# Kernel optimization log

Measured on AMD Instinct MI355X. Metric: run time of the kernel, lower is better.

Reference implementation:

```python
import jax, jax.numpy as jnp
import numpy as np

D_MODEL = 1024; N_HEAD = 16; HD = 64
D_STATE = 128; D_CONV = 4; EXPAND = 2; HEADDIM = 64
D_INNER = EXPAND * D_MODEL          # 2048
NHEADS = D_INNER // HEADDIM         # 32
FFN = 4 * D_MODEL                   # 4096
B, T = 2, 1024


def rmsnorm(x, eps=1e-6):
    # FastSimpleRMSNorm: no learnable weight
    return x * jax.lax.rsqrt(jnp.mean(x * x, axis=-1, keepdims=True) + eps)


def causal_dwconv(x, w, b):
    # x: (..., T, C), w: (C, K), b: (C,). Causal depthwise conv (left pad K-1).
    K = w.shape[1]
    t = x.shape[-2]
    pad = [(0, 0)] * (x.ndim - 2) + [(K - 1, 0), (0, 0)]
    xp = jnp.pad(x, pad)
    y = jnp.zeros_like(x) + b
    for k in range(K):
        y = y + w[:, k] * jax.lax.slice_in_dim(xp, k, k + t, axis=-2)
    return y


def block_forward(x, W_in, conv_w, conv_b, A_log, Dm, dt_bias, mnorm_w, W_out,
                  W_qkv, W_cproj, qconv_w, qconv_b, kconv_w, kconv_b, vconv_w, vconv_b,
                  time_maa_k, time_maa_r, W_key, W_rec, W_val):
    Bsz, Tn, _ = x.shape
    # ---- Mamba2 branch ----
    h = rmsnorm(x)
    zxbcdt = h @ W_in                                  # (B,T,2*D_INNER+2*N+H)
    z = zxbcdt[..., :D_INNER]
    xBC = zxbcdt[..., D_INNER:2 * D_INNER + 2 * D_STATE]
    dt = zxbcdt[..., -NHEADS:]
    xBC = jax.nn.silu(causal_dwconv(xBC, conv_w, conv_b))
    xm = xBC[..., :D_INNER]
    Bm = xBC[..., D_INNER:D_INNER + D_STATE]           # (B,T,N)
    Cm = xBC[..., -D_STATE:]                           # (B,T,N)
    dt = jax.nn.softplus(dt + dt_bias)                 # (B,T,H)
    A = -jnp.exp(A_log)                                # (H,)
    xh = xm.reshape(Bsz, Tn, NHEADS, HEADDIM)          # (B,T,H,P)

    def step(hstate, inp):
        dt_t, x_t, B_t, C_t = inp                      # (B,H),(B,H,P),(B,N),(B,N)
        dA = jnp.exp(dt_t * A)                         # (B,H)
        hstate = hstate * dA[..., None, None] + (dt_t[..., None] * x_t)[..., None] * B_t[:, None, None, :]
        y_t = jnp.einsum('bhpn,bn->bhp', hstate, C_t)
        return hstate, y_t

    h0 = jnp.zeros((Bsz, NHEADS, HEADDIM, D_STATE), x.dtype)
    _, ys = jax.lax.scan(step, h0, (jnp.swapaxes(dt, 0, 1), jnp.swapaxes(xh, 0, 1),
                                    jnp.swapaxes(Bm, 0, 1), jnp.swapaxes(Cm, 0, 1)))
    y = jnp.swapaxes(ys, 0, 1) + xh * Dm[:, None]      # (B,T,H,P)
    y = y.reshape(Bsz, Tn, D_INNER) * jax.nn.silu(z)   # gated
    y = y * jax.lax.rsqrt(jnp.mean(y * y, axis=-1, keepdims=True) + 1e-5) * mnorm_w
    x = x + y @ W_out

    # ---- MQA with depthwise convs ----
    h = rmsnorm(x)
    qkv = h @ W_qkv                                    # (B,T,D_MODEL+2*HD)
    q = qkv[..., :D_MODEL].reshape(Bsz, Tn, N_HEAD, HD).transpose(0, 2, 1, 3)  # (B,H,T,D)
    k = qkv[..., D_MODEL:D_MODEL + HD]                 # (B,T,D) single kv head
    v = qkv[..., -HD:]
    q = causal_dwconv(q, qconv_w, qconv_b)
    k = causal_dwconv(k, kconv_w, kconv_b)
    v = causal_dwconv(v, vconv_w, vconv_b)
    scores = jnp.einsum('bhtd,bsd->bhts', q, k) / np.float32(np.sqrt(HD))
    mask = jnp.tril(jnp.ones((Tn, Tn), bool))
    scores = jnp.where(mask, scores, -jnp.inf)
    p = jax.nn.softmax(scores, axis=-1)
    y = jnp.einsum('bhts,bsd->bhtd', p, v)
    y = y.transpose(0, 2, 1, 3).reshape(Bsz, Tn, D_MODEL)
    x = x + y @ W_cproj

    # ---- RWKV CMix FFN ----
    h = rmsnorm(x)
    xx = jnp.pad(h, ((0, 0), (1, 0), (0, 0)))[:, :Tn] - h   # time_shift(x) - x
    xk = h + xx * time_maa_k
    xr = h + xx * time_maa_r
    kf = jnp.square(jax.nn.relu(xk @ W_key))           # ReLU^2
    kv = kf @ W_val
    x = x + jax.nn.sigmoid(xr @ W_rec) * kv
    return x


def setup_inputs() -> dict:
    key = jax.random.key(0)
    ks = jax.random.split(key, 16)
    def w(k, shape, sc=0.02):
        return jax.random.normal(k, shape, jnp.float32) * sc
    x = jax.random.normal(ks[0], (B, T, D_MODEL), jnp.float32)
    W_in = w(ks[1], (D_MODEL, 2 * D_INNER + 2 * D_STATE + NHEADS))
    conv_w = w(ks[2], (D_INNER + 2 * D_STATE, D_CONV), 0.2)
    conv_b = jnp.zeros((D_INNER + 2 * D_STATE,), jnp.float32)
    A_log = jnp.log(jnp.arange(1, NHEADS + 1, dtype=jnp.float32))
    Dm = jnp.ones((NHEADS,), jnp.float32)
    dt_bias = w(ks[3], (NHEADS,), 0.5)
    mnorm_w = jnp.ones((D_INNER,), jnp.float32)
    W_out = w(ks[4], (D_INNER, D_MODEL))
    W_qkv = w(ks[5], (D_MODEL, D_MODEL + 2 * HD))
    W_cproj = w(ks[6], (D_MODEL, D_MODEL))
    qconv_w = w(ks[7], (HD, 3), 0.3); qconv_b = jnp.zeros((HD,), jnp.float32)
    kconv_w = w(ks[8], (HD, 3), 0.3); kconv_b = jnp.zeros((HD,), jnp.float32)
    vconv_w = w(ks[9], (HD, 3), 0.3); vconv_b = jnp.zeros((HD,), jnp.float32)
    ddd = jnp.arange(D_MODEL, dtype=jnp.float32) / D_MODEL
    time_maa_k = 1.0 - ddd  # layer_id=0 -> ratio_1_to_almost0 = 1
    time_maa_r = 1.0 - ddd
    W_key = w(ks[10], (D_MODEL, FFN))
    W_rec = w(ks[11], (D_MODEL, D_MODEL))
    W_val = w(ks[12], (FFN, D_MODEL))
    return dict(x=x, W_in=W_in, conv_w=conv_w, conv_b=conv_b, A_log=A_log, Dm=Dm,
                dt_bias=dt_bias, mnorm_w=mnorm_w, W_out=W_out, W_qkv=W_qkv, W_cproj=W_cproj,
                qconv_w=qconv_w, qconv_b=qconv_b, kconv_w=kconv_w, kconv_b=kconv_b,
                vconv_w=vconv_w, vconv_b=vconv_b, time_maa_k=time_maa_k, time_maa_r=time_maa_r,
                W_key=W_key, W_rec=W_rec, W_val=W_val)


def reference(x, W_in, conv_w, conv_b, A_log, Dm, dt_bias, mnorm_w, W_out,
              W_qkv, W_cproj, qconv_w, qconv_b, kconv_w, kconv_b, vconv_w, vconv_b,
              time_maa_k, time_maa_r, W_key, W_rec, W_val):
    return block_forward(x, W_in, conv_w, conv_b, A_log, Dm, dt_bias, mnorm_w, W_out,
                         W_qkv, W_cproj, qconv_w, qconv_b, kconv_w, kconv_b, vconv_w, vconv_b,
                         time_maa_k, time_maa_r, W_key, W_rec, W_val)
```

## Files before the change

kernel.cpp:

```cpp
#include <hip/hip_runtime.h>
#include <hip/hip_bf16.h>
#include <math.h>

#define BB 2
#define TT 1024
#define BT (BB*TT)
#define DM 1024
#define DI 2048
#define DS 128
#define NHS 32
#define PDIM 64
#define NHA 16
#define HD 64
#define FFN_ 4096
#define NZX 4384
#define NXBC 2304
#define NXBCD 2336
#define CL 128
#define NC 8

typedef __hip_bfloat16 bf16;
typedef short bf16x8 __attribute__((ext_vector_type(8)));
typedef float f32x4 __attribute__((ext_vector_type(4)));

__device__ __forceinline__ float b2f(bf16 v){ return __bfloat162float(v); }
__device__ __forceinline__ bf16 f2b(float v){ return __float2bfloat16(v); }

__device__ __forceinline__ void gload16(const void* g, void* l) {
  __builtin_amdgcn_global_load_lds(
      (const __attribute__((address_space(1))) unsigned int*)g,
      (__attribute__((address_space(3))) unsigned int*)l,
      16, 0, 0);
}

__global__ void k_rms_in(const float* __restrict__ xin, float* __restrict__ X,
                         bf16* __restrict__ H) {
  int row = blockIdx.x;
  int tid = threadIdx.x;
  const float* xr = xin + (size_t)row * DM;
  float v[4]; float ss = 0.f;
  #pragma unroll
  for (int i = 0; i < 4; ++i) { v[i] = xr[tid*4+i]; ss += v[i]*v[i]; }
  __shared__ float red[256];
  red[tid] = ss; __syncthreads();
  for (int s = 128; s > 0; s >>= 1) { if (tid < s) red[tid] += red[tid+s]; __syncthreads(); }
  float scale = rsqrtf(red[0]/(float)DM + 1e-6f);
  float* Xr = X + (size_t)row*DM; bf16* Hr = H + (size_t)row*DM;
  #pragma unroll
  for (int i = 0; i < 4; ++i) { Xr[tid*4+i] = v[i]; Hr[tid*4+i] = f2b(v[i]*scale); }
}

__global__ void k_rms_f32(const float* __restrict__ X, bf16* __restrict__ H) {
  int row = blockIdx.x;
  int tid = threadIdx.x;
  const float* xr = X + (size_t)row * DM;
  float v[4]; float ss = 0.f;
  #pragma unroll
  for (int i = 0; i < 4; ++i) { v[i] = xr[tid*4+i]; ss += v[i]*v[i]; }
  __shared__ float red[256];
  red[tid] = ss; __syncthreads();
  for (int s = 128; s > 0; s >>= 1) { if (tid < s) red[tid] += red[tid+s]; __syncthreads(); }
  float scale = rsqrtf(red[0]/(float)DM + 1e-6f);
  bf16* Hr = H + (size_t)row*DM;
  #pragma unroll
  for (int i = 0; i < 4; ++i) Hr[tid*4+i] = f2b(v[i]*scale);
}

__global__ void k_rms_shift(const float* __restrict__ X, const float* __restrict__ maak,
                            const float* __restrict__ maar,
                            bf16* __restrict__ XK, bf16* __restrict__ XR) {
  int row = blockIdx.x; int t = row & (TT - 1);
  int tid = threadIdx.x;
  const float* xr = X + (size_t)row*DM;
  const float* xp = xr - DM;
  float v[4], pv[4]; float ss = 0.f, ssp = 0.f;
  #pragma unroll
  for (int i = 0; i < 4; ++i) {
    int c = tid*4 + i;
    v[i] = xr[c]; ss += v[i]*v[i];
    pv[i] = (t > 0) ? xp[c] : 0.f; ssp += pv[i]*pv[i];
  }
  __shared__ float red[256], red2[256];
  red[tid] = ss; red2[tid] = ssp; __syncthreads();
  for (int s = 128; s > 0; s >>= 1) {
    if (tid < s) { red[tid] += red[tid+s]; red2[tid] += red2[tid+s]; }
    __syncthreads();
  }
  float scale  = rsqrtf(red[0]/(float)DM + 1e-6f);
  float scalep = (t > 0) ? rsqrtf(red2[0]/(float)DM + 1e-6f) : 0.f;
  bf16* xk = XK + (size_t)row*DM; bf16* xrw = XR + (size_t)row*DM;
  #pragma unroll
  for (int i = 0; i < 4; ++i) {
    int c = tid*4 + i;
    float h = v[i]*scale;
    float xx = pv[i]*scalep - h;
    xk[c]  = f2b(h + xx*maak[c]);
    xrw[c] = f2b(h + xx*maar[c]);
  }
}

__global__ void k_tcast(const float* __restrict__ W, bf16* __restrict__ Wt,
                        int K, int N) {
  __shared__ float t[32][33];
  int tx = threadIdx.x, ty = threadIdx.y;
  int n0 = blockIdx.x*32, k0 = blockIdx.y*32;
  #pragma unroll
  for (int i = 0; i < 4; ++i) {
    int k = k0 + ty + i*8, n = n0 + tx;
    t[ty + i*8][tx] = (n < N) ? W[(size_t)k*N + n] : 0.f;
  }
  __syncthreads();
  #pragma unroll
  for (int i = 0; i < 4; ++i) {
    int n = n0 + ty + i*8, k = k0 + tx;
    Wt[(size_t)n*K + k] = f2b(t[tx][ty + i*8]);
  }
}

template<int EPI, bool ADD, bool OUTBF>
__global__ __launch_bounds__(256)
void mfma_gemm(const bf16* __restrict__ A, const bf16* __restrict__ Bt,
               float* __restrict__ C, bf16* __restrict__ Cbf,
               int M, int N, int K) {
  __shared__ bf16 As[128*32];
  __shared__ bf16 Bs[128*32];
  int tid = threadIdx.x;
  int wave = tid >> 6, lane = tid & 63;
  int m_l = lane & 15, quad = lane >> 4;
  int wr = (wave & 1) * 64, wc = (wave >> 1) * 64;
  int row0 = blockIdx.y * 128, col0 = blockIdx.x * 128;
  f32x4 acc[4][4];
  #pragma unroll
  for (int i = 0; i < 4; ++i)
    #pragma unroll
    for (int j = 0; j < 4; ++j) acc[i][j] = (f32x4){0.f,0.f,0.f,0.f};
  int lr = lane >> 2;
  int lc = (lane & 3) * 8;
  for (int k0 = 0; k0 < K; k0 += 32) {
    __syncthreads();
    #pragma unroll
    for (int g = 0; g < 2; ++g) {
      int rbase = 32*wave + 16*g;
      gload16(&A [(size_t)(row0 + rbase + lr)*K + k0 + lc], &As[rbase*32]);
      gload16(&Bt[(size_t)(col0 + rbase + lr)*K + k0 + lc], &Bs[rbase*32]);
    }
    __syncthreads();
    bf16x8 af[4], bfv[4];
    #pragma unroll
    for (int i = 0; i < 4; ++i) af[i]  = *(const bf16x8*)&As[(wr + i*16 + m_l)*32 + quad*8];
    #pragma unroll
    for (int j = 0; j < 4; ++j) bfv[j] = *(const bf16x8*)&Bs[(wc + j*16 + m_l)*32 + quad*8];
    #pragma unroll
    for (int i = 0; i < 4; ++i)
      #pragma unroll
      for (int j = 0; j < 4; ++j)
        acc[i][j] = __builtin_amdgcn_mfma_f32_16x16x32_bf16(af[i], bfv[j], acc[i][j], 0, 0, 0);
  }
  #pragma unroll
  for (int i = 0; i < 4; ++i) {
    #pragma unroll
    for (int j = 0; j < 4; ++j) {
      int col = col0 + wc + j*16 + m_l;
      if (col < N) {
        #pragma unroll
        for (int r = 0; r < 4; ++r) {
          int row = row0 + wr + i*16 + quad*4 + r;
          float v = acc[i][j][r];
          if (EPI == 1) { v = fmaxf(v, 0.f); v = v*v; }
          else if (EPI == 2) v = 1.f/(1.f + __expf(-v));
          if (OUTBF)      Cbf[(size_t)row*N + col] = f2b(v);
          else if (ADD)   C[(size_t)row*N + col] += v;
          else            C[(size_t)row*N + col]  = v;
        }
      }
    }
  }
}

__global__ __launch_bounds__(256)
void mfma_sk32(const bf16* __restrict__ A, const bf16* __restrict__ Bt,
               float* __restrict__ P0, float* __restrict__ P1,
               float* __restrict__ P2, float* __restrict__ P3,
               int M, int N, int K, int kchunk) {
  __shared__ bf16 As[128*32];
  __shared__ bf16 Bs[128*32];
  int tid = threadIdx.x;
  int wave = tid >> 6, lane = tid & 63;
  int m_l = lane & 15, quad = lane >> 4;
  int wr = (wave & 1) * 64, wc = (wave >> 1) * 64;
  int row0 = blockIdx.y * 128, col0 = blockIdx.x * 128;
  int kbeg = blockIdx.z * kchunk;
  int kend = kbeg + kchunk;
  f32x4 acc[4][4];
  #pragma unroll
  for (int i = 0; i < 4; ++i)
    #pragma unroll
    for (int j = 0; j < 4; ++j) acc[i][j] = (f32x4){0.f,0.f,0.f,0.f};
  int lr = lane >> 2;
  int lc = (lane & 3) * 8;
  for (int k0 = kbeg; k0 < kend; k0 += 32) {
    __syncthreads();
    #pragma unroll
    for (int g = 0; g < 2; ++g) {
      int rbase = 32*wave + 16*g;
      gload16(&A [(size_t)(row0 + rbase + lr)*K + k0 + lc], &As[rbase*32]);
      gload16(&Bt[(size_t)(col0 + rbase + lr)*K + k0 + lc], &Bs[rbase*32]);
    }
    __syncthreads();
    bf16x8 af[4], bfv[4];
    #pragma unroll
    for (int i = 0; i < 4; ++i) af[i]  = *(const bf16x8*)&As[(wr + i*16 + m_l)*32 + quad*8];
    #pragma unroll
    for (int j = 0; j < 4; ++j) bfv[j] = *(const bf16x8*)&Bs[(wc + j*16 + m_l)*32 + quad*8];
    #pragma unroll
    for (int i = 0; i < 4; ++i)
      #pragma unroll
      for (int j = 0; j < 4; ++j)
        acc[i][j] = __builtin_amdgcn_mfma_f32_16x16x32_bf16(af[i], bfv[j], acc[i][j], 0, 0, 0);
  }
  float* P = (blockIdx.z == 0) ? P0 : (blockIdx.z == 1) ? P1 : (blockIdx.z == 2) ? P2 : P3;
  #pragma unroll
  for (int i = 0; i < 4; ++i) {
    #pragma unroll
    for (int j = 0; j < 4; ++j) {
      int col = col0 + wc + j*16 + m_l;
      if (col < N) {
        #pragma unroll
        for (int r = 0; r < 4; ++r) {
          int row = row0 + wr + i*16 + quad*4 + r;
          P[(size_t)row*N + col] = acc[i][j][r];
        }
      }
    }
  }
}

template<int Z, int EPI, bool ADD>
__global__ void k_reduce(float* __restrict__ dst, const float* __restrict__ p0,
                         const float* __restrict__ p1, const float* __restrict__ p2,
                         const float* __restrict__ p3) {
  size_t i = ((size_t)blockIdx.x*256 + threadIdx.x)*4;
  float4 a = *(const float4*)(p0 + i);
  float4 b = *(const float4*)(p1 + i);
  float r0 = a.x + b.x, r1 = a.y + b.y, r2 = a.z + b.z, r3 = a.w + b.w;
  if (Z == 4) {
    float4 c = *(const float4*)(p2 + i);
    float4 d = *(const float4*)(p3 + i);
    r0 += c.x + d.x; r1 += c.y + d.y; r2 += c.z + d.z; r3 += c.w + d.w;
  }
  if (EPI == 2) {
    r0 = 1.f/(1.f + __expf(-r0)); r1 = 1.f/(1.f + __expf(-r1));
    r2 = 1.f/(1.f + __expf(-r2)); r3 = 1.f/(1.f + __expf(-r3));
  }
  if (ADD) {
    float4 o = *(const float4*)(dst + i);
    r0 += o.x; r1 += o.y; r2 += o.z; r3 += o.w;
  }
  float4 res; res.x = r0; res.y = r1; res.z = r2; res.w = r3;
  *(float4*)(dst + i) = res;
}

__global__ void k_reduce_final(const float* __restrict__ p0, const float* __restrict__ p1,
                               const float* __restrict__ X, const float* __restrict__ KV,
                               float* __restrict__ out) {
  size_t i = ((size_t)blockIdx.x*256 + threadIdx.x)*4;
  float4 a = *(const float4*)(p0 + i);
  float4 b = *(const float4*)(p1 + i);
  float4 x = *(const float4*)(X + i);
  float4 kv = *(const float4*)(KV + i);
  float r0 = 1.f/(1.f + __expf(-(a.x + b.x)));
  float r1 = 1.f/(1.f + __expf(-(a.y + b.y)));
  float r2 = 1.f/(1.f + __expf(-(a.z + b.z)));
  float r3 = 1.f/(1.f + __expf(-(a.w + b.w)));
  float4 res;
  res.x = x.x + r0*kv.x; res.y = x.y + r1*kv.y;
  res.z = x.z + r2*kv.z; res.w = x.w + r3*kv.w;
  *(float4*)(out + i) = res;
}

__global__ void k_conv_ssm(const float* __restrict__ ZXr, const float* __restrict__ cw,
                           const float* __restrict__ cb, const float* __restrict__ dtb,
                           bf16* __restrict__ XBCb, float* __restrict__ DT) {
  int bt = blockIdx.x; int b = bt >> 10; int t = bt & 1023;
  int tid = threadIdx.x;
  for (int c = tid; c < NXBC; c += 256) {
    float acc = cb[c];
    #pragma unroll
    for (int kk = 0; kk < 4; ++kk) {
      int ts = t - 3 + kk;
      if (ts >= 0) acc += cw[c*4+kk] * ZXr[((size_t)(b*TT+ts))*NXBCD + c];
    }
    float s = acc / (1.f + __expf(-acc));
    XBCb[(size_t)bt*NXBC + c] = f2b(s);
  }
  if (tid < NHS) {
    float x = ZXr[(size_t)bt*NXBCD + NXBC + tid] + dtb[tid];
    float sp = (x > 20.f) ? x : log1pf(__expf(x));
    DT[(size_t)bt*NHS + tid] = sp;
  }
}

__global__ __launch_bounds__(512)
void k_scan1(const bf16* __restrict__ xbcb, const float* __restrict__ dt,
             const float* __restrict__ A_log, const float* __restrict__ Dmv,
             float* __restrict__ Y, float* __restrict__ SC, float* __restrict__ CUM) {
  int bc = blockIdx.x;
  int bh = bc >> 3, c = bc & 7;
  int b = bh >> 5, h = bh & 31;
  int tid = threadIdx.x, wave = tid >> 6, lane = tid & 63;
  int col = lane & 15, quad = lane >> 4;
  int t0 = c * CL;
  __shared__ bf16 sB[128*136];
  __shared__ bf16 sC[128*136];
  __shared__ bf16 sxT[64*136];
  __shared__ float sL[128], sdt[128], sW[128];
  float A = -__expf(A_log[h]);
  float Dmh = Dmv[h];
  for (int e = tid; e < 128*16; e += 512) {
    int r = e >> 4, ch = e & 15;
    const bf16* row = xbcb + (size_t)(b*TT + t0 + r)*NXBC;
    *(uint4*)&sB[r*136 + ch*8] = *(const uint4*)&row[2048 + ch*8];
    *(uint4*)&sC[r*136 + ch*8] = *(const uint4*)&row[2176 + ch*8];
  }
  for (int e = tid; e < 64*128; e += 512) {
    int p = e & 63, t = e >> 6;
    sxT[p*136 + t] = xbcb[(size_t)(b*TT + t0 + t)*NXBC + h*64 + p];
  }
  if (tid < 128) sdt[tid] = dt[(size_t)(b*TT + t0 + tid)*NHS + h];
  __syncthreads();
  if (wave == 0) {
    float a0 = sdt[2*lane]*A, a1 = sdt[2*lane+1]*A;
    float tot = a0 + a1;
    #pragma unroll
    for (int off = 1; off < 64; off <<= 1) {
      float up = __shfl_up(tot, off);
      if (lane >= off) tot += up;
    }
    sL[2*lane+1] = tot;
    sL[2*lane]   = tot - a1;
  }
  __syncthreads();
  int wr = (wave & 1)*64, wc = (wave >> 1)*32;
  f32x4 g[4][2];
  #pragma unroll
  for (int i = 0; i < 4; ++i)
    #pragma unroll
    for (int j = 0; j < 2; ++j) g[i][j] = (f32x4){0.f,0.f,0.f,0.f};
  #pragma unroll
  for (int kf = 0; kf < 4; ++kf) {
    bf16x8 af[4], bfr[2];
    #pragma unroll
    for (int i = 0; i < 4; ++i) af[i]  = *(const bf16x8*)&sC[(wr + i*16 + col)*136 + kf*32 + quad*8];
    #pragma unroll
    for (int j = 0; j < 2; ++j) bfr[j] = *(const bf16x8*)&sB[(wc + j*16 + col)*136 + kf*32 + quad*8];
    #pragma unroll
    for (int i = 0; i < 4; ++i)
      #pragma unroll
      for (int j = 0; j < 2; ++j)
        g[i][j] = __builtin_amdgcn_mfma_f32_16x16x32_bf16(af[i], bfr[j], g[i][j], 0, 0, 0);
  }
  float Lend = sL[127];
  if (tid < 128) sW[tid] = __expf(Lend - sL[tid]) * sdt[tid];
  __syncthreads();
  if (tid < 128) CUM[(size_t)bh*TT + t0 + tid] = __expf(sL[tid]);
  #pragma unroll
  for (int i = 0; i < 4; ++i) {
    #pragma unroll
    for (int j = 0; j < 2; ++j) {
      int sl = wc + j*16 + col;
      #pragma unroll
      for (int r = 0; r < 4; ++r) {
        int tl = wr + i*16 + quad*4 + r;
        float v = (sl <= tl) ? g[i][j][r] * __expf(sL[tl] - sL[sl]) * sdt[sl] : 0.f;
        sC[tl*136 + sl] = f2b(v);
      }
    }
  }
  for (int e = tid; e < 128*128; e += 512) {
    int n = e & 127, s = e >> 7;
    sB[n*136 + s] = f2b(b2f(xbcb[(size_t)(b*TT + t0 + s)*NXBC + 2048 + n]) * sW[s]);
  }
  __syncthreads();
  int tb = (wave & 3)*32, pb = (wave >> 2)*32;
  f32x4 ya[2][2];
  #pragma unroll
  for (int i2 = 0; i2 < 2; ++i2)
    #pragma unroll
    for (int jd = 0; jd < 2; ++jd) ya[i2][jd] = (f32x4){0.f,0.f,0.f,0.f};
  #pragma unroll
  for (int kf = 0; kf < 4; ++kf) {
    bf16x8 pa[2], xa[2];
    #pragma unroll
    for (int i2 = 0; i2 < 2; ++i2)
      pa[i2] = *(const bf16x8*)&sC[(tb + i2*16 + col)*136 + kf*32 + quad*8];
    #pragma unroll
    for (int jd = 0; jd < 2; ++jd)
      xa[jd] = *(const bf16x8*)&sxT[(pb + jd*16 + col)*136 + kf*32 + quad*8];
    #pragma unroll
    for (int i2 = 0; i2 < 2; ++i2)
      #pragma unroll
      for (int jd = 0; jd < 2; ++jd)
        ya[i2][jd] = __builtin_amdgcn_mfma_f32_16x16x32_bf16(pa[i2], xa[jd], ya[i2][jd], 0, 0, 0);
  }
  #pragma unroll
  for (int i2 = 0; i2 < 2; ++i2) {
    #pragma unroll
    for (int jd = 0; jd < 2; ++jd) {
      int p = pb + jd*16 + col;
      #pragma unroll
      for (int r = 0; r < 4; ++r) {
        int tl = tb + i2*16 + quad*4 + r;
        float xv = b2f(sxT[p*136 + tl]);
        Y[(size_t)(b*TT + t0 + tl)*DI + h*64 + p] = ya[i2][jd][r] + xv*Dmh;
      }
    }
  }
  int pb3 = (wave & 3)*16, nb = (wave >> 2)*64;
  f32x4 sa[4];
  #pragma unroll
  for (int nt = 0; nt < 4; ++nt) sa[nt] = (f32x4){0.f,0.f,0.f,0.f};
  #pragma unroll
  for (int kf = 0; kf < 4; ++kf) {
    bf16x8 xpa = *(const bf16x8*)&sxT[(pb3 + col)*136 + kf*32 + quad*8];
    #pragma unroll
    for (int nt = 0; nt < 4; ++nt) {
      bf16x8 bwa = *(const bf16x8*)&sB[(nb + nt*16 + col)*136 + kf*32 + quad*8];
      sa[nt] = __builtin_amdgcn_mfma_f32_16x16x32_bf16(xpa, bwa, sa[nt], 0, 0, 0);
    }
  }
  #pragma unroll
  for (int nt = 0; nt < 4; ++nt) {
    int n = nb + nt*16 + col;
    #pragma unroll
    for (int r = 0; r < 4; ++r) {
      int p = pb3 + quad*4 + r;
      SC[((size_t)(bh*NC + c)*64 + p)*128 + n] = sa[nt][r];
    }
  }
}

__global__ __launch_bounds__(512)
void k_scan2(float* __restrict__ SC, const float* __restrict__ CUM) {
  int bh = blockIdx.x;
  int tid = threadIdx.x;
  int p = tid >> 3, g = tid & 7;
  float S[16];
  #pragma unroll
  for (int j = 0; j < 16; ++j) S[j] = 0.f;
  for (int c = 0; c < NC; ++c) {
    size_t base = ((size_t)(bh*NC + c)*64 + p)*128 + g*16;
    float Ptot = CUM[(size_t)bh*TT + c*CL + (CL-1)];
    float tmp[16];
    #pragma unroll
    for (int j = 0; j < 16; ++j) tmp[j] = SC[base + j];
    #pragma unroll
    for (int j = 0; j < 16; ++j) SC[base + j] = S[j];
    #pragma unroll
    for (int j = 0; j < 16; ++j) S[j] = S[j]*Ptot + tmp[j];
  }
}

__global__ __launch_bounds__(256)
void k_scan3(const bf16* __restrict__ xbcb, const float* __restrict__ SC,
             const float* __restrict__ CUM, float* __restrict__ Y) {
  int bc = blockIdx.x;
  int bh = bc >> 3, c = bc & 7;
  if (c == 0) return;
  int b = bh >> 5, h = bh & 31;
  int tid = threadIdx.x, wave = tid >> 6, lane = tid & 63;
  int col = lane & 15, quad = lane >> 4;
  int t0 = c * CL;
  __shared__ bf16 sCt[128*136];
  __shared__ bf16 sS[64*136];
  __shared__ float sCum[128];
  for (int e = tid; e < 128*16; e += 256) {
    int r = e >> 4, ch = e & 15;
    *(uint4*)&sCt[r*136 + ch*8] =
      *(const uint4*)&xbcb[(size_t)(b*TT + t0 + r)*NXBC + 2176 + ch*8];
  }
  for (int e = tid; e < 64*128; e += 256) {
    int n = e & 127, p = e >> 7;
    sS[p*136 + n] = f2b(SC[((size_t)(bh*NC + c)*64 + p)*128 + n]);
  }
  if (tid < 128) sCum[tid] = CUM[(size_t)bh*TT + t0 + tid];
  __syncthreads();
  f32x4 ya[2][4];
  #pragma unroll
  for (int i2 = 0; i2 < 2; ++i2)
    #pragma unroll
    for (int jd = 0; jd < 4; ++jd) ya[i2][jd] = (f32x4){0.f,0.f,0.f,0.f};
  #pragma unroll
  for (int kf = 0; kf < 4; ++kf) {
    bf16x8 pa[2], sv[4];
    #pragma unroll
    for (int i2 = 0; i2 < 2; ++i2)
      pa[i2] = *(const bf16x8*)&sCt[(wave*32 + i2*16 + col)*136 + kf*32 + quad*8];
    #pragma unroll
    for (int jd = 0; jd < 4; ++jd)
      sv[jd] = *(const bf16x8*)&sS[(jd*16 + col)*136 + kf*32 + quad*8];
    #pragma unroll
    for (int i2 = 0; i2 < 2; ++i2)
      #pragma unroll
      for (int jd = 0; jd < 4; ++jd)
        ya[i2][jd] = __builtin_amdgcn_mfma_f32_16x16x32_bf16(pa[i2], sv[jd], ya[i2][jd], 0, 0, 0);
  }
  #pragma unroll
  for (int i2 = 0; i2 < 2; ++i2) {
    #pragma unroll
    for (int jd = 0; jd < 4; ++jd) {
      int p = jd*16 + col;
      #pragma unroll
      for (int r = 0; r < 4; ++r) {
        int tl = wave*32 + i2*16 + quad*4 + r;
        Y[(size_t)(b*TT + t0 + tl)*DI + h*64 + p] += sCum[tl]*ya[i2][jd][r];
      }
    }
  }
}

__global__ void k_gate(const float* __restrict__ Y, const float* __restrict__ Z,
                       const float* __restrict__ mnw, bf16* __restrict__ Ybf) {
  int row = blockIdx.x; int tid = threadIdx.x;
  const float* yr = Y + (size_t)row*DI;
  const float* zr = Z + (size_t)row*DI;
  float gv[8]; float ss = 0.f;
  #pragma unroll
  for (int i = 0; i < 8; ++i) {
    int c = tid*8 + i;
    float z = zr[c];
    float sz = z / (1.f + __expf(-z));
    float v = yr[c]*sz;
    gv[i] = v; ss += v*v;
  }
  __shared__ float red[256];
  red[tid] = ss; __syncthreads();
  for (int s = 128; s > 0; s >>= 1) { if (tid < s) red[tid] += red[tid+s]; __syncthreads(); }
  float scale = rsqrtf(red[0]/(float)DI + 1e-5f);
  bf16* br = Ybf + (size_t)row*DI;
  #pragma unroll
  for (int i = 0; i < 8; ++i) { int c = tid*8 + i; br[c] = f2b(gv[i]*scale*mnw[c]); }
}

__global__ void k_conv_qkv(const float* __restrict__ QKV,
                           const float* qw, const float* qb, const float* kw, const float* kb,
                           const float* vw, const float* vb,
                           bf16* __restrict__ Qb, bf16* __restrict__ Kb, bf16* __restrict__ Vtb) {
  int bt = blockIdx.x; int b = bt >> 10; int t = bt & 1023;
  int tid = threadIdx.x;
  for (int c = tid; c < 1152; c += 256) {
    if (c < 1024) {
      int h = c >> 6, d = c & 63;
      float acc = qb[d];
      #pragma unroll
      for (int kk = 0; kk < 3; ++kk) { int ts = t-2+kk; if (ts >= 0) acc += qw[d*3+kk] * QKV[((size_t)(b*TT+ts))*1152 + c]; }
      Qb[((size_t)(b*NHA + h)*TT + t)*HD + d] = f2b(acc * 0.125f);
    } else if (c < 1088) {
      int d = c - 1024;
      float acc = kb[d];
      #pragma unroll
      for (int kk = 0; kk < 3; ++kk) { int ts = t-2+kk; if (ts >= 0) acc += kw[d*3+kk] * QKV[((size_t)(b*TT+ts))*1152 + c]; }
      Kb[(size_t)bt*HD + d] = f2b(acc);
    } else {
      int d = c - 1088;
      float acc = vb[d];
      #pragma unroll
      for (int kk = 0; kk < 3; ++kk) { int ts = t-2+kk; if (ts >= 0) acc += vw[d*3+kk] * QKV[((size_t)(b*TT+ts))*1152 + c]; }
      Vtb[((size_t)(b*HD + d))*TT + t] = f2b(acc);
    }
  }
}

__global__ __launch_bounds__(256)
void k_flash(const bf16* __restrict__ Qb, const bf16* __restrict__ Kb,
             const bf16* __restrict__ Vtb, bf16* __restrict__ out) {
  int qt = blockIdx.x, h = blockIdx.y, b = blockIdx.z;
  int tid = threadIdx.x, wave = tid >> 6, lane = tid & 63;
  int col = lane & 15, quad = lane >> 4;
  int t0 = qt * 128;
  __shared__ bf16 Ks[128*72];
  __shared__ bf16 Vs[64*136];
  __shared__ bf16 Ps[4][32*136];
  const bf16* Qbase = Qb + ((size_t)(b*NHA + h))*TT*HD;
  bf16x8 qf[2][2];
  #pragma unroll
  for (int i = 0; i < 2; ++i)
    #pragma unroll
    for (int kf = 0; kf < 2; ++kf)
      qf[i][kf] = *(const bf16x8*)&Qbase[(size_t)(t0 + wave*32 + i*16 + col)*HD + kf*32 + quad*8];
  float lst[2][4];
  f32x4 oacc[2][4];
  #pragma unroll
  for (int i = 0; i < 2; ++i)
    #pragma unroll
    for (int r = 0; r < 4; ++r) lst[i][r] = 0.f;
  #pragma unroll
  for (int i = 0; i < 2; ++i)
    #pragma unroll
    for (int jd = 0; jd < 4; ++jd) oacc[i][jd] = (f32x4){0.f,0.f,0.f,0.f};

  for (int kt = 0; kt <= qt; ++kt) {
    int s0 = kt * 128;
    __syncthreads();
    for (int e = tid; e < 1024; e += 256) {
      int r = e >> 3, ch = e & 7;
      *(uint4*)&Ks[r*72 + ch*8] = *(const uint4*)&Kb[((size_t)(b*TT + s0 + r))*HD + ch*8];
    }
    for (int e = tid; e < 1024; e += 256) {
      int d = e >> 4, ch = e & 15;
      *(uint4*)&Vs[d*136 + ch*8] = *(const uint4*)&Vtb[((size_t)(b*HD + d))*TT + s0 + ch*8];
    }
    __syncthreads();
    f32x4 sacc[2][8];
    #pragma unroll
    for (int i = 0; i < 2; ++i)
      #pragma unroll
      for (int j = 0; j < 8; ++j) sacc[i][j] = (f32x4){0.f,0.f,0.f,0.f};
    __builtin_amdgcn_s_setprio(1);
    #pragma unroll
    for (int j = 0; j < 8; ++j) {
      bf16x8 kf0 = *(const bf16x8*)&Ks[(j*16 + col)*72 + quad*8];
      bf16x8 kf1 = *(const bf16x8*)&Ks[(j*16 + col)*72 + 32 + quad*8];
      #pragma unroll
      for (int i = 0; i < 2; ++i) {
        sacc[i][j] = __builtin_amdgcn_mfma_f32_16x16x32_bf16(qf[i][0], kf0, sacc[i][j], 0, 0, 0);
        sacc[i][j] = __builtin_amdgcn_mfma_f32_16x16x32_bf16(qf[i][1], kf1, sacc[i][j], 0, 0, 0);
      }
    }
    __builtin_amdgcn_s_setprio(0);
    bool diag = (kt == qt);
    #pragma unroll
    for (int i = 0; i < 2; ++i) {
      #pragma unroll
      for (int r = 0; r < 4; ++r) {
        int rowloc = wave*32 + i*16 + quad*4 + r;
        #pragma unroll
        for (int j = 0; j < 8; ++j) {
          float pv = __expf(sacc[i][j][r]);
          if (diag && (j*16 + col > rowloc)) pv = 0.f;
          sacc[i][j][r] = pv;
          lst[i][r] += pv;
        }
      }
    }
    #pragma unroll
    for (int i = 0; i < 2; ++i)
      #pragma unroll
      for (int j = 0; j < 8; ++j)
        #pragma unroll
        for (int r = 0; r < 4; ++r)
          Ps[wave][(i*16 + quad*4 + r)*136 + j*16 + col] = f2b(sacc[i][j][r]);
    __builtin_amdgcn_s_setprio(1);
    #pragma unroll
    for (int i = 0; i < 2; ++i) {
      bf16x8 pa[4];
      #pragma unroll
      for (int kf = 0; kf < 4; ++kf)
        pa[kf] = *(const bf16x8*)&Ps[wave][(i*16 + col)*136 + kf*32 + quad*8];
      #pragma unroll
      for (int jd = 0; jd < 4; ++jd) {
        #pragma unroll
        for (int kf = 0; kf < 4; ++kf) {
          bf16x8 vbf = *(const bf16x8*)&Vs[(jd*16 + col)*136 + kf*32 + quad*8];
          oacc[i][jd] = __builtin_amdgcn_mfma_f32_16x16x32_bf16(pa[kf], vbf, oacc[i][jd], 0, 0, 0);
        }
      }
    }
    __builtin_amdgcn_s_setprio(0);
  }
  #pragma unroll
  for (int i = 0; i < 2; ++i)
    #pragma unroll
    for (int r = 0; r < 4; ++r) {
      float l = lst[i][r];
      l += __shfl_xor(l, 1);
      l += __shfl_xor(l, 2);
      l += __shfl_xor(l, 4);
      l += __shfl_xor(l, 8);
      lst[i][r] = l;
    }
  #pragma unroll
  for (int i = 0; i < 2; ++i) {
    #pragma unroll
    for (int jd = 0; jd < 4; ++jd) {
      int d = jd*16 + col;
      #pragma unroll
      for (int r = 0; r < 4; ++r) {
        int t = t0 + wave*32 + i*16 + quad*4 + r;
        out[((size_t)(b*TT + t))*DM + h*64 + d] = f2b(oacc[i][jd][r] / lst[i][r]);
      }
    }
  }
}

extern "C" void kernel_launch(void* const* d_in, const int* in_sizes, int n_in,
                              void* d_out, int out_size, void* d_ws, size_t ws_size,
                              hipStream_t stream) {
  const float* x_in    = (const float*)d_in[0];
  const float* W_in    = (const float*)d_in[1];
  const float* conv_w  = (const float*)d_in[2];
  const float* conv_b  = (const float*)d_in[3];
  const float* A_log   = (const float*)d_in[4];
  const float* Dm      = (const float*)d_in[5];
  const float* dt_bias = (const float*)d_in[6];
  const float* mnorm_w = (const float*)d_in[7];
  const float* W_out   = (const float*)d_in[8];
  const float* W_qkv   = (const float*)d_in[9];
  const float* W_cproj = (const float*)d_in[10];
  const float* qconv_w = (const float*)d_in[11];
  const float* qconv_b = (const float*)d_in[12];
  const float* kconv_w = (const float*)d_in[13];
  const float* kconv_b = (const float*)d_in[14];
  const float* vconv_w = (const float*)d_in[15];
  const float* vconv_b = (const float*)d_in[16];
  const float* maa_k   = (const float*)d_in[17];
  const float* maa_r   = (const float*)d_in[18];
  const float* W_key   = (const float*)d_in[19];
  const float* W_rec   = (const float*)d_in[20];
  const float* W_val   = (const float*)d_in[21];
  float* out = (float*)d_out;

  float* ws = (float*)d_ws;
  float* X       = ws;
  bf16*  Hbf     = (bf16*)(ws + 2097152);
  float* Zbuf    = ws + 3145728;
  float* XBCDraw = ws + 7340032;
  float* XBC     = ws + 12124160;
  float* DT      = ws + 16842752;
  float* CUM     = ws + 16908288;
  float* Y       = ws + 16973824;

  bf16*  Wt_in    = (bf16*)XBC;
  bf16*  XBCb     = (bf16*)XBC;
  float* SC       = XBCDraw;
  bf16*  Ybf      = (bf16*)XBC;
  bf16*  Wt_out   = (bf16*)(XBC + 2097152);
  float* QKV      = Zbuf;
  bf16*  Wt_qkv   = (bf16*)XBC;
  bf16*  Qb       = (bf16*)XBCDraw;
  bf16*  Kb       = (bf16*)(XBCDraw + 1048576);
  bf16*  Vtb      = (bf16*)(XBCDraw + 1114112);
  bf16*  ATTNbf   = (bf16*)Y;
  bf16*  Wt_cproj = (bf16*)(Y + 1048576);
  bf16*  XKbf     = (bf16*)XBC;
  bf16*  XRbf     = (bf16*)(XBC + 1048576);
  bf16*  Wt_key   = (bf16*)Zbuf;
  bf16*  KFbf     = (bf16*)XBCDraw;
  bf16*  Wt_val   = (bf16*)Zbuf;
  float* KV       = Y;
  bf16*  Wt_rec   = (bf16*)Zbuf;

  dim3 thr256(256), thr512(512);
  dim3 tblk(32, 8);

  k_rms_in<<<BT, thr256, 0, stream>>>(x_in, X, Hbf);
  k_tcast<<<dim3(4480/32, 1024/32), tblk, 0, stream>>>(W_in, Wt_in, 1024, NZX);
  mfma_gemm<0,false,false><<<dim3(16, 16), thr256, 0, stream>>>(Hbf, Wt_in, Zbuf, nullptr, BT, 2048, 1024);
  mfma_gemm<0,false,false><<<dim3(19, 16), thr256, 0, stream>>>(Hbf, Wt_in + (size_t)2048*1024, XBCDraw, nullptr, BT, NXBCD, 1024);
  k_conv_ssm<<<BT, thr256, 0, stream>>>(XBCDraw, conv_w, conv_b, dt_bias, XBCb, DT);
  k_scan1<<<BB*NHS*NC, thr512, 0, stream>>>(XBCb, DT, A_log, Dm, Y, SC, CUM);
  k_scan2<<<BB*NHS, thr512, 0, stream>>>(SC, CUM);
  k_scan3<<<BB*NHS*NC, thr256, 0, stream>>>(XBCb, SC, CUM, Y);
  k_gate<<<BT, thr256, 0, stream>>>(Y, Zbuf, mnorm_w, Ybf);
  k_tcast<<<dim3(1024/32, 2048/32), tblk, 0, stream>>>(W_out, Wt_out, 2048, 1024);
  mfma_sk32<<<dim3(8, 16, 4), thr256, 0, stream>>>(Ybf, Wt_out,
      Zbuf, Zbuf + 2097152, XBCDraw, XBCDraw + 2097152, BT, 1024, 2048, 512);
  k_reduce<4,0,true><<<2048, thr256, 0, stream>>>(X, Zbuf, Zbuf + 2097152, XBCDraw, XBCDraw + 2097152);
  k_rms_f32<<<BT, thr256, 0, stream>>>(X, Hbf);
  k_tcast<<<dim3(1152/32, 1024/32), tblk, 0, stream>>>(W_qkv, Wt_qkv, 1024, 1152);
  mfma_sk32<<<dim3(9, 16, 2), thr256, 0, stream>>>(Hbf, Wt_qkv,
      XBCDraw, XBCDraw + 2359296, XBCDraw, XBCDraw, BT, 1152, 1024, 512);
  k_reduce<2,0,false><<<2304, thr256, 0, stream>>>(QKV, XBCDraw, XBCDraw + 2359296, XBCDraw, XBCDraw);
  k_conv_qkv<<<BT, thr256, 0, stream>>>(QKV, qconv_w, qconv_b, kconv_w, kconv_b, vconv_w, vconv_b, Qb, Kb, Vtb);
  k_flash<<<dim3(TT/128, NHA, BB), thr256, 0, stream>>>(Qb, Kb, Vtb, ATTNbf);
  k_tcast<<<dim3(1024/32, 1024/32), tblk, 0, stream>>>(W_cproj, Wt_cproj, 1024, 1024);
  mfma_sk32<<<dim3(8, 16, 2), thr256, 0, stream>>>(ATTNbf, Wt_cproj,
      XBC, XBC + 2097152, XBC, XBC, BT, 1024, 1024, 512);
  k_reduce<2,0,true><<<2048, thr256, 0, stream>>>(X, XBC, XBC + 2097152, XBC, XBC);
  k_rms_shift<<<BT, thr256, 0, stream>>>(X, maa_k, maa_r, XKbf, XRbf);
  k_tcast<<<dim3(4096/32, 1024/32), tblk, 0, stream>>>(W_key, Wt_key, 1024, 4096);
  mfma_gemm<1,false,true><<<dim3(32, 16), thr256, 0, stream>>>(XKbf, Wt_key, nullptr, KFbf, BT, 4096, 1024);
  k_tcast<<<dim3(1024/32, 4096/32), tblk, 0, stream>>>(W_val, Wt_val, 4096, 1024);
  mfma_sk32<<<dim3(8, 16, 4), thr256, 0, stream>>>(KFbf, Wt_val,
      Y, Y + 2097152, XBC + 2621440, Zbuf + 2097152, BT, 1024, 4096, 1024);
  k_reduce<4,0,false><<<2048, thr256, 0, stream>>>(KV, Y, Y + 2097152, XBC + 2621440, Zbuf + 2097152);
  k_tcast<<<dim3(1024/32, 1024/32), tblk, 0, stream>>>(W_rec, Wt_rec, 1024, 1024);
  mfma_sk32<<<dim3(8, 16, 2), thr256, 0, stream>>>(XRbf, Wt_rec,
      Y + 2097152, XBC + 2621440, Y, Y, BT, 1024, 1024, 512);
  k_reduce_final<<<2048, thr256, 0, stream>>>(Y + 2097152, XBC + 2621440, X, KV, out);
}
```

Baseline: 548.4 us.

## Split causal flash attention KV range across two blocks and combine partials

Result: no change. 541.3 us (-1.3%).

```diff
diff --git a/kernel.cpp b/kernel.cpp
--- a/kernel.cpp
+++ b/kernel.cpp
@@ -571,9 +571,15 @@
 }
 
 __global__ __launch_bounds__(256)
-void k_flash(const bf16* __restrict__ Qb, const bf16* __restrict__ Kb,
-             const bf16* __restrict__ Vtb, bf16* __restrict__ out) {
-  int qt = blockIdx.x, h = blockIdx.y, b = blockIdx.z;
+void k_flash_sk(const bf16* __restrict__ Qb, const bf16* __restrict__ Kb,
+                const bf16* __restrict__ Vtb, float* __restrict__ Op,
+                float* __restrict__ Lp) {
+  int qt = blockIdx.x >> 1, z = blockIdx.x & 1;
+  int h = blockIdx.y, b = blockIdx.z;
+  int n = qt + 1;
+  int kmid = (n + 1) >> 1;
+  int kbeg = z ? kmid : 0;
+  int kend = z ? n : kmid;
   int tid = threadIdx.x, wave = tid >> 6, lane = tid & 63;
   int col = lane & 15, quad = lane >> 4;
   int t0 = qt * 128;
@@ -581,12 +587,6 @@
   __shared__ bf16 Vs[64*136];
   __shared__ bf16 Ps[4][32*136];
   const bf16* Qbase = Qb + ((size_t)(b*NHA + h))*TT*HD;
-  bf16x8 qf[2][2];
-  #pragma unroll
-  for (int i = 0; i < 2; ++i)
-    #pragma unroll
-    for (int kf = 0; kf < 2; ++kf)
-      qf[i][kf] = *(const bf16x8*)&Qbase[(size_t)(t0 + wave*32 + i*16 + col)*HD + kf*32 + quad*8];
   float lst[2][4];
   f32x4 oacc[2][4];
   #pragma unroll
@@ -597,87 +597,97 @@
   for (int i = 0; i < 2; ++i)
     #pragma unroll
     for (int jd = 0; jd < 4; ++jd) oacc[i][jd] = (f32x4){0.f,0.f,0.f,0.f};
-
-  for (int kt = 0; kt <= qt; ++kt) {
-    int s0 = kt * 128;
-    __syncthreads();
-    for (int e = tid; e < 1024; e += 256) {
-      int r = e >> 3, ch = e & 7;
-      *(uint4*)&Ks[r*72 + ch*8] = *(const uint4*)&Kb[((size_t)(b*TT + s0 + r))*HD + ch*8];
-    }
-    for (int e = tid; e < 1024; e += 256) {
-      int d = e >> 4, ch = e & 15;
-      *(uint4*)&Vs[d*136 + ch*8] = *(const uint4*)&Vtb[((size_t)(b*HD + d))*TT + s0 + ch*8];
-    }
-    __syncthreads();
-    f32x4 sacc[2][8];
+  if (kbeg < kend) {
+    bf16x8 qf[2][2];
     #pragma unroll
     for (int i = 0; i < 2; ++i)
       #pragma unroll
-      for (int j = 0; j < 8; ++j) sacc[i][j] = (f32x4){0.f,0.f,0.f,0.f};
-    __builtin_amdgcn_s_setprio(1);
-    #pragma unroll
-    for (int j = 0; j < 8; ++j) {
-      bf16x8 kf0 = *(const bf16x8*)&Ks[(j*16 + col)*72 + quad*8];
-      bf16x8 kf1 = *(const bf16x8*)&Ks[(j*16 + col)*72 + 32 + quad*8];
+      for (int kf = 0; kf < 2; ++kf)
+        qf[i][kf] = *(const bf16x8*)&Qbase[(size_t)(t0 + wave*32 + i*16 + col)*HD + kf*32 + quad*8];
+
+    for (int kt = kbeg; kt < kend; ++kt) {
+      int s0 = kt * 128;
+      __syncthreads();
+      for (int e = tid; e < 1024; e += 256) {
+        int r = e >> 3, ch = e & 7;
+        *(uint4*)&Ks[r*72 + ch*8] = *(const uint4*)&Kb[((size_t)(b*TT + s0 + r))*HD + ch*8];
+      }
+      for (int e = tid; e < 1024; e += 256) {
+        int d = e >> 4, ch = e & 15;
+        *(uint4*)&Vs[d*136 + ch*8] = *(const uint4*)&Vtb[((size_t)(b*HD + d))*TT + s0 + ch*8];
+      }
+      __syncthreads();
+      f32x4 sacc[2][8];
+      #pragma unroll
+      for (int i = 0; i < 2; ++i)
+        #pragma unroll
+        for (int j = 0; j < 8; ++j) sacc[i][j] = (f32x4){0.f,0.f,0.f,0.f};
+      __builtin_amdgcn_s_setprio(1);
+      #pragma unroll
+      for (int j = 0; j < 8; ++j) {
+        bf16x8 kf0 = *(const bf16x8*)&Ks[(j*16 + col)*72 + quad*8];
+        bf16x8 kf1 = *(const bf16x8*)&Ks[(j*16 + col)*72 + 32 + quad*8];
+        #pragma unroll
+        for (int i = 0; i < 2; ++i) {
+          sacc[i][j] = __builtin_amdgcn_mfma_f32_16x16x32_bf16(qf[i][0], kf0, sacc[i][j], 0, 0, 0);
+          sacc[i][j] = __builtin_amdgcn_mfma_f32_16x16x32_bf16(qf[i][1], kf1, sacc[i][j], 0, 0, 0);
+        }
+      }
+      __builtin_amdgcn_s_setprio(0);
+      bool diag = (kt == qt);
       #pragma unroll
       for (int i = 0; i < 2; ++i) {
-        sacc[i][j] = __builtin_amdgcn_mfma_f32_16x16x32_bf16(qf[i][0], kf0, sacc[i][j], 0, 0, 0);
-        sacc[i][j] = __builtin_amdgcn_mfma_f32_16x16x32_bf16(qf[i][1], kf1, sacc[i][j], 0, 0, 0);
-      }
-    }
-    __builtin_amdgcn_s_setprio(0);
-    bool diag = (kt == qt);
-    #pragma unroll
-    for (int i = 0; i < 2; ++i) {
+        #pragma unroll
+        for (int r = 0; r < 4; ++r) {
+          int rowloc = wave*32 + i*16 + quad*4 + r;
+          #pragma unroll
+          for (int j = 0; j < 8; ++j) {
+            float pv = __expf(sacc[i][j][r]);
+            if (diag && (j*16 + col > rowloc)) pv = 0.f;
+            sacc[i][j][r] = pv;
+            lst[i][r] += pv;
+          }
+        }
+      }
+      #pragma unroll
+      for (int i = 0; i < 2; ++i)
+        #pragma unroll
+        for (int j = 0; j < 8; ++j)
+          #pragma unroll
+          for (int r = 0; r < 4; ++r)
+            Ps[wave][(i*16 + quad*4 + r)*136 + j*16 + col] = f2b(sacc[i][j][r]);
+      __builtin_amdgcn_s_setprio(1);
+      #pragma unroll
+      for (int i = 0; i < 2; ++i) {
+        bf16x8 pa[4];
+        #pragma unroll
+        for (int kf = 0; kf < 4; ++kf)
+          pa[kf] = *(const bf16x8*)&Ps[wave][(i*16 + col)*136 + kf*32 + quad*8];
+        #pragma unroll
+        for (int jd = 0; jd < 4; ++jd) {
+          #pragma unroll
+          for (int kf = 0; kf < 4; ++kf) {
+            bf16x8 vbf = *(const bf16x8*)&Vs[(jd*16 + col)*136 + kf*32 + quad*8];
+            oacc[i][jd] = __builtin_amdgcn_mfma_f32_16x16x32_bf16(pa[kf], vbf, oacc[i][jd], 0, 0, 0);
+          }
+        }
+      }
+      __builtin_amdgcn_s_setprio(0);
+    }
+    #pragma unroll
+    for (int i = 0; i < 2; ++i)
       #pragma unroll
       for (int r = 0; r < 4; ++r) {
-        int rowloc = wave*32 + i*16 + quad*4 + r;
-        #pragma unroll
-        for (int j = 0; j < 8; ++j) {
-          float pv = __expf(sacc[i][j][r]);
-          if (diag && (j*16 + col > rowloc)) pv = 0.f;
-          sacc[i][j][r] = pv;
-          lst[i][r] += pv;
-        }
-      }
-    }
-    #pragma unroll
-    for (int i = 0; i < 2; ++i)
-      #pragma unroll
-      for (int j = 0; j < 8; ++j)
-        #pragma unroll
-        for (int r = 0; r < 4; ++r)
-          Ps[wave][(i*16 + quad*4 + r)*136 + j*16 + col] = f2b(sacc[i][j][r]);
-    __builtin_amdgcn_s_setprio(1);
-    #pragma unroll
-    for (int i = 0; i < 2; ++i) {
-      bf16x8 pa[4];
-      #pragma unroll
-      for (int kf = 0; kf < 4; ++kf)
-        pa[kf] = *(const bf16x8*)&Ps[wave][(i*16 + col)*136 + kf*32 + quad*8];
-      #pragma unroll
-      for (int jd = 0; jd < 4; ++jd) {
-        #pragma unroll
-        for (int kf = 0; kf < 4; ++kf) {
-          bf16x8 vbf = *(const bf16x8*)&Vs[(jd*16 + col)*136 + kf*32 + quad*8];
-          oacc[i][jd] = __builtin_amdgcn_mfma_f32_16x16x32_bf16(pa[kf], vbf, oacc[i][jd], 0, 0, 0);
-        }
-      }
-    }
-    __builtin_amdgcn_s_setprio(0);
-  }
-  #pragma unroll
-  for (int i = 0; i < 2; ++i)
-    #pragma unroll
-    for (int r = 0; r < 4; ++r) {
-      float l = lst[i][r];
-      l += __shfl_xor(l, 1);
-      l += __shfl_xor(l, 2);
-      l += __shfl_xor(l, 4);
-      l += __shfl_xor(l, 8);
-      lst[i][r] = l;
-    }
+        float l = lst[i][r];
+        l += __shfl_xor(l, 1);
+        l += __shfl_xor(l, 2);
+        l += __shfl_xor(l, 4);
+        l += __shfl_xor(l, 8);
+        lst[i][r] = l;
+      }
+  }
+  if (qt == 0 && z == 1) return;
+  size_t robase = ((size_t)((z*BB + b)*NHA + h))*TT + t0;
   #pragma unroll
   for (int i = 0; i < 2; ++i) {
     #pragma unroll
@@ -685,11 +695,42 @@
       int d = jd*16 + col;
       #pragma unroll
       for (int r = 0; r < 4; ++r) {
-        int t = t0 + wave*32 + i*16 + quad*4 + r;
-        out[((size_t)(b*TT + t))*DM + h*64 + d] = f2b(oacc[i][jd][r] / lst[i][r]);
-      }
-    }
-  }
+        int tl = wave*32 + i*16 + quad*4 + r;
+        Op[(robase + tl)*HD + d] = oacc[i][jd][r];
+      }
+    }
+  }
+  if (col == 0) {
+    #pragma unroll
+    for (int i = 0; i < 2; ++i)
+      #pragma unroll
+      for (int r = 0; r < 4; ++r) {
+        int tl = wave*32 + i*16 + quad*4 + r;
+        Lp[robase + tl] = lst[i][r];
+      }
+  }
+}
+
+__global__ void k_att_comb(const float* __restrict__ Op, const float* __restrict__ Lp,
+                           bf16* __restrict__ outb) {
+  int idx = blockIdx.x*256 + threadIdx.x;
+  int e = idx*4;
+  int c = e & (DM - 1); int h = c >> 6; int d = c & 63;
+  int bt = e >> 10; int t = bt & (TT - 1); int b = bt >> 10;
+  int qt = t >> 7;
+  size_t r0 = ((size_t)(b*NHA + h))*TT + t;
+  float4 o0 = *(const float4*)&Op[r0*HD + d];
+  float l = Lp[r0];
+  float ox = o0.x, oy = o0.y, oz = o0.z, ow = o0.w;
+  if (qt > 0) {
+    size_t r1 = ((size_t)((BB + b)*NHA + h))*TT + t;
+    float4 o1 = *(const float4*)&Op[r1*HD + d];
+    l += Lp[r1];
+    ox += o1.x; oy += o1.y; oz += o1.z; ow += o1.w;
+  }
+  float inv = 1.f / l;
+  bf16* p = outb + (size_t)bt*DM + c;
+  p[0] = f2b(ox*inv); p[1] = f2b(oy*inv); p[2] = f2b(oz*inv); p[3] = f2b(ow*inv);
 }
 
 extern "C" void kernel_launch(void* const* d_in, const int* in_sizes, int n_in,
@@ -748,6 +789,8 @@
   bf16*  Wt_val   = (bf16*)Zbuf;
   float* KV       = Y;
   bf16*  Wt_rec   = (bf16*)Zbuf;
+  float* FOp      = Zbuf;
+  float* FLp      = ws + 2097152;
 
   dim3 thr256(256), thr512(512);
   dim3 tblk(32, 8);
@@ -771,7 +814,8 @@
       XBCDraw, XBCDraw + 2359296, XBCDraw, XBCDraw, BT, 1152, 1024, 512);
   k_reduce<2,0,false><<<2304, thr256, 0, stream>>>(QKV, XBCDraw, XBCDraw + 2359296, XBCDraw, XBCDraw);
   k_conv_qkv<<<BT, thr256, 0, stream>>>(QKV, qconv_w, qconv_b, kconv_w, kconv_b, vconv_w, vconv_b, Qb, Kb, Vtb);
-  k_flash<<<dim3(TT/128, NHA, BB), thr256, 0, stream>>>(Qb, Kb, Vtb, ATTNbf);
+  k_flash_sk<<<dim3((TT/128)*2, NHA, BB), thr256, 0, stream>>>(Qb, Kb, Vtb, FOp, FLp);
+  k_att_comb<<<(BT*DM)/(256*4), thr256, 0, stream>>>(FOp, FLp, ATTNbf);
   k_tcast<<<dim3(1024/32, 1024/32), tblk, 0, stream>>>(W_cproj, Wt_cproj, 1024, 1024);
   mfma_sk32<<<dim3(8, 16, 2), thr256, 0, stream>>>(ATTNbf, Wt_cproj,
       XBC, XBC + 2097152, XBC, XBC, BT, 1024, 1024, 512);
```
